# Kernel optimization log

Measured on AMD Instinct MI355X. Metric: run time of the kernel, lower is better.

## Reference

```python
import jax, jax.numpy as jnp
import numpy as np

D_MODEL = 512
NHEAD = 8
HEAD_DIM = D_MODEL // NHEAD  # 64, also rotary_dim
WIN_LO, WIN_HI = 127, 128    # attn_window: kv in [q-127, q+128]
BLOCK = 256                  # block size for banded attention (>= WIN_LO+1 and >= WIN_HI)


def setup_inputs() -> dict:
    key = jax.random.key(0)
    k1, k2, k3, k4 = jax.random.split(key, 4)
    N, T = 4, 2048
    x = jax.random.normal(k1, (N, T, D_MODEL), dtype=jnp.float32)
    Wqkv_w = jax.random.normal(k2, (3 * D_MODEL, D_MODEL), dtype=jnp.float32) * 0.02
    out_w = jax.random.normal(k3, (D_MODEL, D_MODEL), dtype=jnp.float32) * 0.02
    out_b = jax.random.normal(k4, (D_MODEL,), dtype=jnp.float32) * 0.02
    return {"x": x, "Wqkv_w": Wqkv_w, "out_w": out_w, "out_b": out_b}


def _rotate_half(u):
    u1, u2 = jnp.split(u, 2, axis=-1)
    return jnp.concatenate((-u2, u1), axis=-1)


def _apply_rope(q, k, T, dtype):
    # inv_freq: [HEAD_DIM/2]
    inv_freq = 1.0 / (10000.0 ** (jnp.arange(0, HEAD_DIM, 2, dtype=jnp.float32) / HEAD_DIM))
    pos = jnp.arange(T, dtype=dtype)
    freqs = pos[:, None] * inv_freq[None, :].astype(dtype)      # [T, D/2]
    emb = jnp.concatenate((freqs, freqs), axis=-1)              # [T, D]
    cos = jnp.cos(emb)[None, :, None, :]                        # [1,T,1,D]
    sin = jnp.sin(emb)[None, :, None, :]
    q = q * cos + _rotate_half(q) * sin
    k = k * cos + _rotate_half(k) * sin
    return q, k


def reference(x, Wqkv_w, out_w, out_b):
    N, T, dm = x.shape
    H, D, B = NHEAD, HEAD_DIM, BLOCK
    qkv = (x @ Wqkv_w.T).reshape(N, T, 3, H, D)
    q, k, v = qkv[:, :, 0], qkv[:, :, 1], qkv[:, :, 2]          # [N,T,H,D]
    q, k = _apply_rope(q, k, T, x.dtype)
    # [N,H,T,D]
    q = q.transpose(0, 2, 1, 3)
    k = k.transpose(0, 2, 1, 3)
    v = v.transpose(0, 2, 1, 3)

    nb = T // B
    qb = q.reshape(N, H, nb, B, D)
    kb = k.reshape(N, H, nb, B, D)
    vb = v.reshape(N, H, nb, B, D)
    # pad one block of zeros on each side so block g sees key blocks g-1,g,g+1
    pad = ((0, 0), (0, 0), (1, 1), (0, 0), (0, 0))
    kp = jnp.pad(kb, pad)
    vp = jnp.pad(vb, pad)
    # [N,H,nb,3B,D]
    kwin = jnp.concatenate([kp[:, :, i:i + nb] for i in range(3)], axis=3)
    vwin = jnp.concatenate([vp[:, :, i:i + nb] for i in range(3)], axis=3)

    scale = 1.0 / np.sqrt(D)
    scores = jnp.einsum('nhgqd,nhgkd->nhgqk', qb, kwin) * scale  # [N,H,nb,B,3B]

    qi = jnp.arange(B)
    kj = jnp.arange(3 * B)
    gidx = jnp.arange(nb)
    diff = kj[None, None, :] - B - qi[None, :, None]             # [1,B,3B] kv - q offset
    band = (diff >= -WIN_LO) & (diff <= WIN_HI)
    kv_global = gidx[:, None, None] * B + kj[None, None, :] - B  # [nb,1,3B]
    valid = (kv_global >= 0) & (kv_global < T)
    mask = band & valid                                          # [nb,B,3B]

    neg = jnp.asarray(-1e30, dtype=scores.dtype)
    scores = jnp.where(mask[None, None], scores, neg)
    probs = jax.nn.softmax(scores, axis=-1)
    attn = jnp.einsum('nhgqk,nhgkd->nhgqd', probs, vwin)         # [N,H,nb,B,D]
    attn = attn.reshape(N, H, T, D).transpose(0, 2, 1, 3).reshape(N, T, dm)
    return attn @ out_w.T + out_b
```

## Files before the change

### kernel.cpp

```cpp
#include <hip/hip_runtime.h>
#include <math.h>


typedef __attribute__((ext_vector_type(8))) __bf16 bf16x8;
typedef __attribute__((ext_vector_type(4))) float f32x4;

__device__ __forceinline__ unsigned short f2bf(float f) {
    unsigned int u = __float_as_uint(f);
    u += 0x7fffu + ((u >> 16) & 1u);
    return (unsigned short)(u >> 16);
}
__device__ __forceinline__ unsigned int packbf2(float a, float b) {
    unsigned int ua = __float_as_uint(a); ua += 0x7fffu + ((ua >> 16) & 1u);
    unsigned int ub = __float_as_uint(b); ub += 0x7fffu + ((ub >> 16) & 1u);
    return (ua >> 16) | (ub & 0xffff0000u);
}
__device__ __forceinline__ bf16x8 as_bf16x8(uint4 u) {
    union { uint4 u4; bf16x8 v; } c; c.u4 = u; return c.v;
}

__device__ __forceinline__ void async16(void* lds, const void* g) {
    __builtin_amdgcn_global_load_lds(
        (const __attribute__((address_space(1))) void*)g,
        (__attribute__((address_space(3))) void*)lds,
        16, 0, 0);
}

__global__ __launch_bounds__(256) void cvt_all(
    const float* __restrict__ x, const float* __restrict__ w1,
    const float* __restrict__ w2,
    unsigned short* __restrict__ xb, unsigned short* __restrict__ w1b,
    unsigned short* __restrict__ w2b)
{
    const int n_x  = 8192 * 512 / 4;
    const int n_w1 = 1536 * 512 / 4;
    const int n_w2 = 512 * 512 / 4;
    int i = blockIdx.x * 256 + threadIdx.x;
    const float* in; unsigned short* out; int j;
    if (i < n_x)                  { in = x;  out = xb;  j = i; }
    else if (i < n_x + n_w1)      { in = w1; out = w1b; j = i - n_x; }
    else if (i < n_x + n_w1 + n_w2) { in = w2; out = w2b; j = i - n_x - n_w1; }
    else return;
    float4 v = *(const float4*)(in + 4 * (size_t)j);
    uint2 o;
    o.x = packbf2(v.x, v.y);
    o.y = packbf2(v.z, v.w);
    *(uint2*)(out + 4 * (size_t)j) = o;
}

__global__ __launch_bounds__(256) void gemm_bt_mfma(
    const unsigned short* __restrict__ A, const unsigned short* __restrict__ B,
    const float* __restrict__ bias, void* __restrict__ Cout,
    int M, int O, int K, int write_bf16, int do_rope)
{
    __shared__ __align__(16) unsigned short As[128 * 32];
    __shared__ __align__(16) unsigned short Bs[128 * 32];

    const int tid  = threadIdx.x;
    const int wave = tid >> 6;
    const int lane = tid & 63;
    const int row0 = blockIdx.x * 128;
    const int col0 = blockIdx.y * 128;
    const int wr   = (wave >> 1) * 64;
    const int wc   = (wave & 1) * 64;

    f32x4 acc[4][4] = {};

    const int r_a  = tid >> 2;
    const int cblk = (tid & 3) * 8;
    const int qk   = (lane >> 4) * 8;
    const int lrow = lane & 15;

    for (int k0 = 0; k0 < K; k0 += 32) {
        async16(&As[(size_t)tid * 8],         A + (size_t)(row0 + r_a) * K + k0 + cblk);
        async16(&As[(size_t)(tid + 256) * 8], A + (size_t)(row0 + 64 + r_a) * K + k0 + cblk);
        async16(&Bs[(size_t)tid * 8],         B + (size_t)(col0 + r_a) * K + k0 + cblk);
        async16(&Bs[(size_t)(tid + 256) * 8], B + (size_t)(col0 + 64 + r_a) * K + k0 + cblk);
        __syncthreads();

        bf16x8 af[4], bfr[4];
        #pragma unroll
        for (int mt = 0; mt < 4; ++mt)
            af[mt] = as_bf16x8(*(const uint4*)&As[(wr + mt * 16 + lrow) * 32 + qk]);
        #pragma unroll
        for (int nt = 0; nt < 4; ++nt)
            bfr[nt] = as_bf16x8(*(const uint4*)&Bs[(wc + nt * 16 + lrow) * 32 + qk]);

        #pragma unroll
        for (int mt = 0; mt < 4; ++mt)
            #pragma unroll
            for (int nt = 0; nt < 4; ++nt)
                acc[mt][nt] = __builtin_amdgcn_mfma_f32_16x16x32_bf16(
                    af[mt], bfr[nt], acc[mt][nt], 0, 0, 0);
        __syncthreads();
    }

    const int qrow = (lane >> 4) * 4;

    if (do_rope && col0 < 1024) {
        const float cfreq = 0.28782313662425574f;
        const float invf0 = expf(-(float)lrow * cfreq);
        const float invf1 = expf(-(float)(16 + lrow) * cfreq);
        #pragma unroll
        for (int mt = 0; mt < 4; ++mt) {
            #pragma unroll
            for (int r = 0; r < 4; ++r) {
                const int t = (row0 + wr + mt * 16 + qrow + r) & 2047;
                #pragma unroll
                for (int p = 0; p < 2; ++p) {
                    float ang = (float)t * (p ? invf1 : invf0);
                    float s, c;
                    sincosf(ang, &s, &c);
                    float a = acc[mt][p][r];
                    float b = acc[mt][p + 2][r];
                    acc[mt][p][r]     = a * c - b * s;
                    acc[mt][p + 2][r] = b * c + a * s;
                }
            }
        }
        if (col0 < 512) {
            #pragma unroll
            for (int mt = 0; mt < 4; ++mt)
                #pragma unroll
                for (int nt = 0; nt < 4; ++nt)
                    #pragma unroll
                    for (int r = 0; r < 4; ++r)
                        acc[mt][nt][r] *= 0.125f;
        }
    }

    #pragma unroll
    for (int nt = 0; nt < 4; ++nt) {
        const int col = col0 + wc + nt * 16 + lrow;
        const float bv = bias ? bias[col] : 0.f;
        #pragma unroll
        for (int mt = 0; mt < 4; ++mt) {
            const int rowb = row0 + wr + mt * 16 + qrow;
            if (write_bf16) {
                unsigned short* C = (unsigned short*)Cout;
                #pragma unroll
                for (int r = 0; r < 4; ++r)
                    C[(size_t)(rowb + r) * O + col] = f2bf(acc[mt][nt][r] + bv);
            } else {
                float* C = (float*)Cout;
                #pragma unroll
                for (int r = 0; r < 4; ++r)
                    C[(size_t)(rowb + r) * O + col] = acc[mt][nt][r] + bv;
            }
        }
    }
}

__global__ __launch_bounds__(256) void attn_mfma_kernel(
    const unsigned short* __restrict__ qkv, unsigned short* __restrict__ attnout)
{
    __shared__ __align__(16) unsigned short Kt[64 * 72];
    __shared__ __align__(16) unsigned short Vt[64 * 72];
    __shared__ __align__(16) unsigned short Ps[4][16 * 72];

    const int qt = blockIdx.x;
    const int h  = blockIdx.y;
    const int n  = blockIdx.z;
    const int t0 = qt * 64;
    const int tid  = threadIdx.x;
    const int wave = tid >> 6;
    const int lane = tid & 63;
    const int l15  = lane & 15;
    const int lg   = lane >> 4;

    const size_t base = (size_t)n * 2048 * 1536 + (size_t)h * 64;

    bf16x8 qfrag[2];
    {
        const unsigned short* qp = qkv + base + (size_t)(t0 + wave * 16 + l15) * 1536;
        qfrag[0] = as_bf16x8(*(const uint4*)(qp + lg * 8));
        qfrag[1] = as_bf16x8(*(const uint4*)(qp + 32 + lg * 8));
    }

    const int skey = tid >> 2;
    const int sd0  = (tid & 3) * 16;

    float m_r[4], l_r[4];
    #pragma unroll
    for (int r = 0; r < 4; ++r) { m_r[r] = -1e30f; l_r[r] = 0.f; }
    f32x4 acc_o[4] = {};

    for (int dt = -2; dt <= 2; ++dt) {
        const int kt = qt + dt;
        if (kt < 0 || kt > 31) continue;
        const int s0 = kt * 64;

        {
            const unsigned short* kp = qkv + base + 512 + (size_t)(s0 + skey) * 1536 + sd0;
            uint4 k0 = *(const uint4*)kp;
            uint4 k1 = *(const uint4*)(kp + 8);
            *(uint4*)&Kt[skey * 72 + sd0]     = k0;
            *(uint4*)&Kt[skey * 72 + sd0 + 8] = k1;

            const unsigned short* vp = qkv + base + 1024 + (size_t)(s0 + skey) * 1536 + sd0;
            uint4 a = *(const uint4*)vp;
            uint4 b = *(const uint4*)(vp + 8);
            Vt[(sd0 +  0) * 72 + skey] = (unsigned short)(a.x & 0xffffu);
            Vt[(sd0 +  1) * 72 + skey] = (unsigned short)(a.x >> 16);
            Vt[(sd0 +  2) * 72 + skey] = (unsigned short)(a.y & 0xffffu);
            Vt[(sd0 +  3) * 72 + skey] = (unsigned short)(a.y >> 16);
            Vt[(sd0 +  4) * 72 + skey] = (unsigned short)(a.z & 0xffffu);
            Vt[(sd0 +  5) * 72 + skey] = (unsigned short)(a.z >> 16);
            Vt[(sd0 +  6) * 72 + skey] = (unsigned short)(a.w & 0xffffu);
            Vt[(sd0 +  7) * 72 + skey] = (unsigned short)(a.w >> 16);
            Vt[(sd0 +  8) * 72 + skey] = (unsigned short)(b.x & 0xffffu);
            Vt[(sd0 +  9) * 72 + skey] = (unsigned short)(b.x >> 16);
            Vt[(sd0 + 10) * 72 + skey] = (unsigned short)(b.y & 0xffffu);
            Vt[(sd0 + 11) * 72 + skey] = (unsigned short)(b.y >> 16);
            Vt[(sd0 + 12) * 72 + skey] = (unsigned short)(b.z & 0xffffu);
            Vt[(sd0 + 13) * 72 + skey] = (unsigned short)(b.z >> 16);
            Vt[(sd0 + 14) * 72 + skey] = (unsigned short)(b.w & 0xffffu);
            Vt[(sd0 + 15) * 72 + skey] = (unsigned short)(b.w >> 16);
        }
        __syncthreads();

        f32x4 acc_s[4] = {};
        #pragma unroll
        for (int kstep = 0; kstep < 2; ++kstep) {
            #pragma unroll
            for (int nt = 0; nt < 4; ++nt) {
                bf16x8 kf = as_bf16x8(
                    *(const uint4*)&Kt[(nt * 16 + l15) * 72 + kstep * 32 + lg * 8]);
                acc_s[nt] = __builtin_amdgcn_mfma_f32_16x16x32_bf16(
                    qfrag[kstep], kf, acc_s[nt], 0, 0, 0);
            }
        }

        float sc[4][4];
        #pragma unroll
        for (int nt = 0; nt < 4; ++nt) {
            const int key_off = dt * 64 + nt * 16 + l15;
            #pragma unroll
            for (int r = 0; r < 4; ++r) {
                const int diff = key_off - (wave * 16 + lg * 4 + r);
                const bool ok = (diff >= -127) && (diff <= 128);
                sc[nt][r] = ok ? acc_s[nt][r] : -1e30f;
            }
        }
        #pragma unroll
        for (int r = 0; r < 4; ++r) {
            float tm = fmaxf(fmaxf(sc[0][r], sc[1][r]), fmaxf(sc[2][r], sc[3][r]));
            tm = fmaxf(tm, __shfl_xor(tm, 1, 64));
            tm = fmaxf(tm, __shfl_xor(tm, 2, 64));
            tm = fmaxf(tm, __shfl_xor(tm, 4, 64));
            tm = fmaxf(tm, __shfl_xor(tm, 8, 64));
            const float m_new = fmaxf(m_r[r], tm);
            const float alpha = expf(m_r[r] - m_new);
            float psum = 0.f;
            #pragma unroll
            for (int nt = 0; nt < 4; ++nt) {
                float p = expf(sc[nt][r] - m_new);
                sc[nt][r] = p;
                psum += p;
            }
            psum += __shfl_xor(psum, 1, 64);
            psum += __shfl_xor(psum, 2, 64);
            psum += __shfl_xor(psum, 4, 64);
            psum += __shfl_xor(psum, 8, 64);
            l_r[r] = l_r[r] * alpha + psum;
            m_r[r] = m_new;
            #pragma unroll
            for (int nt = 0; nt < 4; ++nt) acc_o[nt][r] *= alpha;
        }

        #pragma unroll
        for (int nt = 0; nt < 4; ++nt)
            #pragma unroll
            for (int r = 0; r < 4; ++r)
                Ps[wave][(lg * 4 + r) * 72 + nt * 16 + l15] = f2bf(sc[nt][r]);

        __syncthreads();

        bf16x8 pfrag[2];
        pfrag[0] = as_bf16x8(*(const uint4*)&Ps[wave][l15 * 72 + lg * 8]);
        pfrag[1] = as_bf16x8(*(const uint4*)&Ps[wave][l15 * 72 + 32 + lg * 8]);

        #pragma unroll
        for (int kstep = 0; kstep < 2; ++kstep) {
            #pragma unroll
            for (int nt = 0; nt < 4; ++nt) {
                bf16x8 vf = as_bf16x8(
                    *(const uint4*)&Vt[(nt * 16 + l15) * 72 + kstep * 32 + lg * 8]);
                acc_o[nt] = __builtin_amdgcn_mfma_f32_16x16x32_bf16(
                    pfrag[kstep], vf, acc_o[nt], 0, 0, 0);
            }
        }
        __syncthreads();
    }

    float inv_l[4];
    #pragma unroll
    for (int r = 0; r < 4; ++r) inv_l[r] = 1.0f / l_r[r];

    #pragma unroll
    for (int r = 0; r < 4; ++r) {
        const int tq = t0 + wave * 16 + lg * 4 + r;
        unsigned short* op = attnout + (size_t)(n * 2048 + tq) * 512 + h * 64;
        #pragma unroll
        for (int nt = 0; nt < 4; ++nt)
            op[nt * 16 + l15] = f2bf(acc_o[nt][r] * inv_l[r]);
    }
}

extern "C" void kernel_launch(void* const* d_in, const int* in_sizes, int n_in,
                              void* d_out, int out_size, void* d_ws, size_t ws_size,
                              hipStream_t stream)
{
    (void)in_sizes; (void)n_in; (void)out_size; (void)ws_size;

    const float* x     = (const float*)d_in[0];
    const float* Wqkv  = (const float*)d_in[1];
    const float* out_w = (const float*)d_in[2];
    const float* out_b = (const float*)d_in[3];
    float* out = (float*)d_out;

    unsigned short* qkvb  = (unsigned short*)d_ws;
    unsigned short* attnb = qkvb + (size_t)8192 * 1536;
    unsigned short* xb    = attnb + (size_t)8192 * 512;
    unsigned short* wqkvb = xb + (size_t)8192 * 512;
    unsigned short* outwb = wqkvb + (size_t)1536 * 512;

    cvt_all<<<5120, 256, 0, stream>>>(x, Wqkv, out_w, xb, wqkvb, outwb);

    gemm_bt_mfma<<<dim3(64, 12), 256, 0, stream>>>(xb, wqkvb, nullptr, qkvb,
                                                   8192, 1536, 512, 1, 1);
    attn_mfma_kernel<<<dim3(32, 8, 4), 256, 0, stream>>>(qkvb, attnb);
    gemm_bt_mfma<<<dim3(64, 4), 256, 0, stream>>>(attnb, outwb, out_b, out,
                                                  8192, 512, 512, 0, 0);
}
```

Baseline: 154.7 us.

## Load GEMM and attention K fragments directly from global, drop LDS staging

The GEMM kernel no longer stages tiles through LDS. Each wave loads its MFMA fragments straight from global memory into registers and prefetches the next k-slice one step ahead, which removes both barriers per iteration. The attention kernel likewise reads K fragments directly from global, dropping the K shared buffer and one barrier. Fast-math __expf/__sincosf replace the precise versions. In exchange, each wave now reads its own tile copies, so there is no cross-wave reuse through LDS, and global traffic and cache pressure rise.

```diff
diff --git a/kernel.cpp b/kernel.cpp
--- a/kernel.cpp
+++ b/kernel.cpp
@@ -18,12 +18,8 @@
 __device__ __forceinline__ bf16x8 as_bf16x8(uint4 u) {
     union { uint4 u4; bf16x8 v; } c; c.u4 = u; return c.v;
 }
-
-__device__ __forceinline__ void async16(void* lds, const void* g) {
-    __builtin_amdgcn_global_load_lds(
-        (const __attribute__((address_space(1))) void*)g,
-        (__attribute__((address_space(3))) void*)lds,
-        16, 0, 0);
+__device__ __forceinline__ bf16x8 ld_frag(const unsigned short* p) {
+    return as_bf16x8(*(const uint4*)p);
 }
 
 __global__ __launch_bounds__(256) void cvt_all(
@@ -37,8 +33,8 @@
     const int n_w2 = 512 * 512 / 4;
     int i = blockIdx.x * 256 + threadIdx.x;
     const float* in; unsigned short* out; int j;
-    if (i < n_x)                  { in = x;  out = xb;  j = i; }
-    else if (i < n_x + n_w1)      { in = w1; out = w1b; j = i - n_x; }
+    if (i < n_x)                    { in = x;  out = xb;  j = i; }
+    else if (i < n_x + n_w1)        { in = w1; out = w1b; j = i - n_x; }
     else if (i < n_x + n_w1 + n_w2) { in = w2; out = w2b; j = i - n_x - n_w1; }
     else return;
     float4 v = *(const float4*)(in + 4 * (size_t)j);
@@ -48,69 +44,70 @@
     *(uint2*)(out + 4 * (size_t)j) = o;
 }
 
-__global__ __launch_bounds__(256) void gemm_bt_mfma(
+__global__ __launch_bounds__(256) void gemm_bt_direct(
     const unsigned short* __restrict__ A, const unsigned short* __restrict__ B,
     const float* __restrict__ bias, void* __restrict__ Cout,
     int M, int O, int K, int write_bf16, int do_rope)
 {
-    __shared__ __align__(16) unsigned short As[128 * 32];
-    __shared__ __align__(16) unsigned short Bs[128 * 32];
-
     const int tid  = threadIdx.x;
     const int wave = tid >> 6;
     const int lane = tid & 63;
-    const int row0 = blockIdx.x * 128;
-    const int col0 = blockIdx.y * 128;
-    const int wr   = (wave >> 1) * 64;
-    const int wc   = (wave & 1) * 64;
+    const int l15  = lane & 15;
+    const int lg   = lane >> 4;
+
+    const int row0 = blockIdx.x * 128 + (wave >> 1) * 64;
+    const int col0 = blockIdx.y * 128 + (wave & 1) * 64;
+
+    const unsigned short* pa = A + (size_t)(row0 + l15) * K + lg * 8;
+    const unsigned short* pb = B + (size_t)(col0 + l15) * K + lg * 8;
+    const size_t mstride = (size_t)16 * K;
 
     f32x4 acc[4][4] = {};
 
-    const int r_a  = tid >> 2;
-    const int cblk = (tid & 3) * 8;
-    const int qk   = (lane >> 4) * 8;
-    const int lrow = lane & 15;
-
-    for (int k0 = 0; k0 < K; k0 += 32) {
-        async16(&As[(size_t)tid * 8],         A + (size_t)(row0 + r_a) * K + k0 + cblk);
-        async16(&As[(size_t)(tid + 256) * 8], A + (size_t)(row0 + 64 + r_a) * K + k0 + cblk);
-        async16(&Bs[(size_t)tid * 8],         B + (size_t)(col0 + r_a) * K + k0 + cblk);
-        async16(&Bs[(size_t)(tid + 256) * 8], B + (size_t)(col0 + 64 + r_a) * K + k0 + cblk);
-        __syncthreads();
-
-        bf16x8 af[4], bfr[4];
-        #pragma unroll
-        for (int mt = 0; mt < 4; ++mt)
-            af[mt] = as_bf16x8(*(const uint4*)&As[(wr + mt * 16 + lrow) * 32 + qk]);
-        #pragma unroll
-        for (int nt = 0; nt < 4; ++nt)
-            bfr[nt] = as_bf16x8(*(const uint4*)&Bs[(wc + nt * 16 + lrow) * 32 + qk]);
-
+    bf16x8 a_cur[4], b_cur[4];
+    #pragma unroll
+    for (int mt = 0; mt < 4; ++mt) a_cur[mt] = ld_frag(pa + mt * mstride);
+    #pragma unroll
+    for (int nt = 0; nt < 4; ++nt) b_cur[nt] = ld_frag(pb + nt * mstride);
+
+    const int iters = K >> 5;
+    for (int it = 0; it < iters; ++it) {
+        bf16x8 a_nxt[4], b_nxt[4];
+        if (it + 1 < iters) {
+            const int k0 = (it + 1) * 32;
+            #pragma unroll
+            for (int mt = 0; mt < 4; ++mt) a_nxt[mt] = ld_frag(pa + mt * mstride + k0);
+            #pragma unroll
+            for (int nt = 0; nt < 4; ++nt) b_nxt[nt] = ld_frag(pb + nt * mstride + k0);
+        }
         #pragma unroll
         for (int mt = 0; mt < 4; ++mt)
             #pragma unroll
             for (int nt = 0; nt < 4; ++nt)
                 acc[mt][nt] = __builtin_amdgcn_mfma_f32_16x16x32_bf16(
-                    af[mt], bfr[nt], acc[mt][nt], 0, 0, 0);
-        __syncthreads();
-    }
-
-    const int qrow = (lane >> 4) * 4;
+                    a_cur[mt], b_cur[nt], acc[mt][nt], 0, 0, 0);
+        #pragma unroll
+        for (int mt = 0; mt < 4; ++mt) a_cur[mt] = a_nxt[mt];
+        #pragma unroll
+        for (int nt = 0; nt < 4; ++nt) b_cur[nt] = b_nxt[nt];
+    }
+
+    const int qrow = lg * 4;
 
     if (do_rope && col0 < 1024) {
         const float cfreq = 0.28782313662425574f;
-        const float invf0 = expf(-(float)lrow * cfreq);
-        const float invf1 = expf(-(float)(16 + lrow) * cfreq);
+        const float invf0 = __expf(-(float)l15 * cfreq);
+        const float invf1 = __expf(-(float)(16 + l15) * cfreq);
         #pragma unroll
         for (int mt = 0; mt < 4; ++mt) {
             #pragma unroll
             for (int r = 0; r < 4; ++r) {
-                const int t = (row0 + wr + mt * 16 + qrow + r) & 2047;
+                const int t = (row0 + mt * 16 + qrow + r) & 2047;
                 #pragma unroll
                 for (int p = 0; p < 2; ++p) {
                     float ang = (float)t * (p ? invf1 : invf0);
                     float s, c;
-                    sincosf(ang, &s, &c);
+                    __sincosf(ang, &s, &c);
                     float a = acc[mt][p][r];
                     float b = acc[mt][p + 2][r];
                     acc[mt][p][r]     = a * c - b * s;
@@ -131,11 +128,11 @@
 
     #pragma unroll
     for (int nt = 0; nt < 4; ++nt) {
-        const int col = col0 + wc + nt * 16 + lrow;
+        const int col = col0 + nt * 16 + l15;
         const float bv = bias ? bias[col] : 0.f;
         #pragma unroll
         for (int mt = 0; mt < 4; ++mt) {
-            const int rowb = row0 + wr + mt * 16 + qrow;
+            const int rowb = row0 + mt * 16 + qrow;
             if (write_bf16) {
                 unsigned short* C = (unsigned short*)Cout;
                 #pragma unroll
@@ -154,7 +151,6 @@
 __global__ __launch_bounds__(256) void attn_mfma_kernel(
     const unsigned short* __restrict__ qkv, unsigned short* __restrict__ attnout)
 {
-    __shared__ __align__(16) unsigned short Kt[64 * 72];
     __shared__ __align__(16) unsigned short Vt[64 * 72];
     __shared__ __align__(16) unsigned short Ps[4][16 * 72];
 
@@ -173,8 +169,8 @@
     bf16x8 qfrag[2];
     {
         const unsigned short* qp = qkv + base + (size_t)(t0 + wave * 16 + l15) * 1536;
-        qfrag[0] = as_bf16x8(*(const uint4*)(qp + lg * 8));
-        qfrag[1] = as_bf16x8(*(const uint4*)(qp + 32 + lg * 8));
+        qfrag[0] = ld_frag(qp + lg * 8);
+        qfrag[1] = ld_frag(qp + 32 + lg * 8);
     }
 
     const int skey = tid >> 2;
@@ -191,12 +187,6 @@
         const int s0 = kt * 64;
 
         {
-            const unsigned short* kp = qkv + base + 512 + (size_t)(s0 + skey) * 1536 + sd0;
-            uint4 k0 = *(const uint4*)kp;
-            uint4 k1 = *(const uint4*)(kp + 8);
-            *(uint4*)&Kt[skey * 72 + sd0]     = k0;
-            *(uint4*)&Kt[skey * 72 + sd0 + 8] = k1;
-
             const unsigned short* vp = qkv + base + 1024 + (size_t)(s0 + skey) * 1536 + sd0;
             uint4 a = *(const uint4*)vp;
             uint4 b = *(const uint4*)(vp + 8);
@@ -217,17 +207,19 @@
             Vt[(sd0 + 14) * 72 + skey] = (unsigned short)(b.w & 0xffffu);
             Vt[(sd0 + 15) * 72 + skey] = (unsigned short)(b.w >> 16);
         }
-        __syncthreads();
 
         f32x4 acc_s[4] = {};
-        #pragma unroll
-        for (int kstep = 0; kstep < 2; ++kstep) {
-            #pragma unroll
-            for (int nt = 0; nt < 4; ++nt) {
-                bf16x8 kf = as_bf16x8(
-                    *(const uint4*)&Kt[(nt * 16 + l15) * 72 + kstep * 32 + lg * 8]);
-                acc_s[nt] = __builtin_amdgcn_mfma_f32_16x16x32_bf16(
-                    qfrag[kstep], kf, acc_s[nt], 0, 0, 0);
+        {
+            const unsigned short* kb = qkv + base + 512 + (size_t)s0 * 1536;
+            #pragma unroll
+            for (int kstep = 0; kstep < 2; ++kstep) {
+                #pragma unroll
+                for (int nt = 0; nt < 4; ++nt) {
+                    bf16x8 kf = ld_frag(kb + (size_t)(nt * 16 + l15) * 1536
+                                           + kstep * 32 + lg * 8);
+                    acc_s[nt] = __builtin_amdgcn_mfma_f32_16x16x32_bf16(
+                        qfrag[kstep], kf, acc_s[nt], 0, 0, 0);
+                }
             }
         }
 
@@ -250,11 +242,11 @@
             tm = fmaxf(tm, __shfl_xor(tm, 4, 64));
             tm = fmaxf(tm, __shfl_xor(tm, 8, 64));
             const float m_new = fmaxf(m_r[r], tm);
-            const float alpha = expf(m_r[r] - m_new);
+            const float alpha = __expf(m_r[r] - m_new);
             float psum = 0.f;
             #pragma unroll
             for (int nt = 0; nt < 4; ++nt) {
-                float p = expf(sc[nt][r] - m_new);
+                float p = __expf(sc[nt][r] - m_new);
                 sc[nt][r] = p;
                 psum += p;
             }
@@ -277,15 +269,14 @@
         __syncthreads();
 
         bf16x8 pfrag[2];
-        pfrag[0] = as_bf16x8(*(const uint4*)&Ps[wave][l15 * 72 + lg * 8]);
-        pfrag[1] = as_bf16x8(*(const uint4*)&Ps[wave][l15 * 72 + 32 + lg * 8]);
+        pfrag[0] = ld_frag(&Ps[wave][l15 * 72 + lg * 8]);
+        pfrag[1] = ld_frag(&Ps[wave][l15 * 72 + 32 + lg * 8]);
 
         #pragma unroll
         for (int kstep = 0; kstep < 2; ++kstep) {
             #pragma unroll
             for (int nt = 0; nt < 4; ++nt) {
-                bf16x8 vf = as_bf16x8(
-                    *(const uint4*)&Vt[(nt * 16 + l15) * 72 + kstep * 32 + lg * 8]);
+                bf16x8 vf = ld_frag(&Vt[(nt * 16 + l15) * 72 + kstep * 32 + lg * 8]);
                 acc_o[nt] = __builtin_amdgcn_mfma_f32_16x16x32_bf16(
                     pfrag[kstep], vf, acc_o[nt], 0, 0, 0);
             }
@@ -327,9 +318,9 @@
 
     cvt_all<<<5120, 256, 0, stream>>>(x, Wqkv, out_w, xb, wqkvb, outwb);
 
-    gemm_bt_mfma<<<dim3(64, 12), 256, 0, stream>>>(xb, wqkvb, nullptr, qkvb,
-                                                   8192, 1536, 512, 1, 1);
+    gemm_bt_direct<<<dim3(64, 12), 256, 0, stream>>>(xb, wqkvb, nullptr, qkvb,
+                                                     8192, 1536, 512, 1, 1);
     attn_mfma_kernel<<<dim3(32, 8, 4), 256, 0, stream>>>(qkvb, attnb);
-    gemm_bt_mfma<<<dim3(64, 4), 256, 0, stream>>>(attnb, outwb, out_b, out,
-                                                  8192, 512, 512, 0, 0);
-}
+    gemm_bt_direct<<<dim3(64, 4), 256, 0, stream>>>(attnb, outwb, out_b, out,
+                                                    8192, 512, 512, 0, 0);
+}
```

Result: slower. 173.3 us (+12.0%).
